# Kernel optimization log

Hardware: AMD Instinct MI355X
Metric: run time of the kernel (lower is better)

Reference implementation:

```python
import jax, jax.numpy as jnp
import numpy as np

HEADS = 8
DIM = 32  # dim_heads


def setup_inputs() -> dict:
    key = jax.random.key(0)
    k1, k2, k3, k4 = jax.random.split(key, 4)
    b, c, h, w = 8, 256, 128, 128
    hidden = HEADS * DIM  # 256
    x = jax.random.normal(k1, (b, c, h, w), dtype=jnp.float32)
    w_qkv = jax.random.normal(k2, (3 * hidden, c), dtype=jnp.float32) * 0.05
    w_out = jax.random.normal(k3, (c, hidden), dtype=jnp.float32) * 0.05
    b_out = jax.random.normal(k4, (c,), dtype=jnp.float32) * 0.05
    return {"x": x, "w_qkv": w_qkv, "w_out": w_out, "b_out": b_out}


def reference(x, w_qkv, w_out, b_out):
    b, c, h, w = x.shape
    n = h * w
    # 1x1 conv == channel matmul: [b, 3*heads*dim, h, w]
    qkv = jnp.einsum('bchw,oc->bohw', x, w_qkv)
    # rearrange 'b (qkv heads c) h w -> qkv b heads c (h w)'
    qkv = qkv.reshape(b, 3, HEADS, DIM, n)
    q, k, v = qkv[:, 0], qkv[:, 1], qkv[:, 2]  # each [b, heads, dim, n]
    k = jax.nn.softmax(k, axis=-1)
    # context: [b, heads, dim, dim]
    context = jnp.einsum('bhdn,bhen->bhde', k, v)
    o = jnp.einsum('bhde,bhdn->bhen', context, q)  # [b, heads, dim, n]
    o = o.reshape(b, HEADS * DIM, h, w)
    # out 1x1 conv with bias
    o = jnp.einsum('bchw,oc->bohw', o, w_out) + b_out[None, :, None, None]
    return o
```

## Files before the change

kernel.cpp:

```cpp
#include <hip/hip_runtime.h>
#include <hip/hip_bf16.h>
#include <cstdint>

#define NPIX 16384
#define BATCH 8
#define CDIM 256

typedef __bf16 bh8 __attribute__((ext_vector_type(8)));
typedef __bf16 bh4 __attribute__((ext_vector_type(4)));
typedef float  fx4 __attribute__((ext_vector_type(4)));

__device__ __forceinline__ void gload16(const void* g, void* l) {
  __builtin_amdgcn_global_load_lds(
      (const __attribute__((address_space(1))) uint32_t*)g,
      (__attribute__((address_space(3))) uint32_t*)l, 16, 0, 0);
}

__device__ __forceinline__ fx4 mfma16(bh8 a, bh8 b, fx4 c) {
  return __builtin_amdgcn_mfma_f32_16x16x32_bf16(a, b, c, 0, 0, 0);
}

__device__ __forceinline__ void pbar() {
  asm volatile("" ::: "memory");
  __builtin_amdgcn_s_barrier();
  asm volatile("" ::: "memory");
}
#define VMWI(n) asm volatile("s_waitcnt vmcnt(" #n ")" ::: "memory")

__global__ __launch_bounds__(256) void prep_w(const float* __restrict__ w_qkv,
                                              __bf16* __restrict__ wqb,
                                              __bf16* __restrict__ wqT) {
  __shared__ float tile[32][33];
  int bid = blockIdx.x;
  if (bid < 512) {
    int i = bid * 256 + threadIdx.x;
    wqb[i] = (__bf16)w_qkv[256 * 256 + i];
  } else {
    bid -= 512;
    const int t0 = (bid & 7) * 32, o0 = (bid >> 3) * 32;
    const int tx = threadIdx.x & 31, ty = threadIdx.x >> 5;
#pragma unroll
    for (int j = 0; j < 4; ++j) {
      int r = ty * 4 + j;
      tile[r][tx] = w_qkv[(size_t)(o0 + r) * 256 + t0 + tx];
    }
    __syncthreads();
#pragma unroll
    for (int j = 0; j < 4; ++j) {
      int tl = ty * 4 + j;
      wqT[(size_t)(t0 + tl) * 256 + o0 + tx] = (__bf16)tile[tx][tl];
    }
  }
}

__global__ __launch_bounds__(256) void transpose_x(const float* __restrict__ x,
                                                   __bf16* __restrict__ xT) {
  __shared__ float tf[64][68];
  const int n0 = blockIdx.x * 64, c0 = blockIdx.y * 64, b = blockIdx.z;
  const int u = threadIdx.x;
#pragma unroll
  for (int i = 0; i < 4; ++i) {
    int j = i * 256 + u;
    int r = j >> 4, q = j & 15;
    *(fx4*)&tf[r][q * 4] =
        *(const fx4*)&x[((size_t)b * CDIM + c0 + r) * NPIX + n0 + q * 4];
  }
  __syncthreads();
  const int nl = u >> 2, cq = (u & 3) * 16;
#pragma unroll
  for (int w = 0; w < 2; ++w) {
    bh8 v;
#pragma unroll
    for (int j = 0; j < 8; ++j) v[j] = (__bf16)tf[cq + w * 8 + j][nl];
    *(bh8*)&xT[((size_t)b * NPIX + n0 + nl) * CDIM + c0 + cq + w * 8] = v;
  }
}


#define BSP(pb) ((__bf16*)(smem + 32768 + (pb)*16384))

#define STA(kt)                                                                \
  do {                                                                         \
    _Pragma("unroll") for (int i_ = 0; i_ < 4; ++i_) {                         \
      int j_ = i_ * 512 + tid;                                                 \
      int row_ = j_ >> 3, c_ = j_ & 7;                                         \
      int sc_ = c_ ^ (row_ & 7);                                               \
      const __bf16* sb_;                                                       \
      if (EPI == 0) sb_ = (i_ < 2) ? Abk + (size_t)row_ * 256                  \
                                   : Abv + (size_t)(row_ - 128) * 256;         \
      else          sb_ = Ab + (size_t)row_ * 256;                             \
      gload16(sb_ + (kt)*64 + sc_ * 8, As + j_ * 8);                           \
    }                                                                          \
  } while (0)

#define STB(kt, pb)                                                            \
  do {                                                                         \
    _Pragma("unroll") for (int i_ = 0; i_ < 2; ++i_) {                         \
      int j_ = i_ * 512 + tid;                                                 \
      int row_ = j_ >> 3, c_ = j_ & 7;                                         \
      int sc_ = c_ ^ (row_ & 7);                                               \
      gload16(Bb + (size_t)row_ * 256 + (kt)*64 + sc_ * 8, BSP(pb) + j_ * 8);  \
    }                                                                          \
  } while (0)

#define COMP(pb)                                                               \
  do {                                                                         \
    _Pragma("unroll") for (int ks_ = 0; ks_ < 2; ++ks_) {                      \
      bh8 a_[4], b_[4];                                                        \
      const int swk_ = (ks_ * 4 + fq) ^ (fr & 7);                              \
      _Pragma("unroll") for (int m_ = 0; m_ < 4; ++m_)                         \
        a_[m_] = *(const bh8*)&As[(wm * 64 + m_ * 16 + fr) * 64 + swk_ * 8];   \
      _Pragma("unroll") for (int n_ = 0; n_ < 4; ++n_)                         \
        b_[n_] = *(const bh8*)&BSP(pb)[(wn * 64 + n_ * 16 + fr) * 64 + swk_ * 8];\
      _Pragma("unroll") for (int m_ = 0; m_ < 4; ++m_)                         \
      _Pragma("unroll") for (int n_ = 0; n_ < 4; ++n_)                         \
        acc[m_][n_] = mfma16(a_[m_], b_[n_], acc[m_][n_]);                     \
    }                                                                          \
  } while (0)

template <int EPI>
__global__ __launch_bounds__(512, 4) void gemm256(
    const __bf16* __restrict__ A, const __bf16* __restrict__ Bx,
    float* __restrict__ S_part, float* __restrict__ Zpart,
    const float* __restrict__ bias, float* __restrict__ fout) {
  __shared__ __align__(16) char smem[66560];
  __bf16* As = (__bf16*)smem;
  const int tid = threadIdx.x;
  const int bx = (EPI == 0) ? blockIdx.y : blockIdx.x;
  const int by = (EPI == 0) ? blockIdx.x : blockIdx.y;
  const int b = blockIdx.z;
  const int lane = tid & 63, wid = tid >> 6;
  const int wm = wid >> 1, wn = wid & 1;
  const int fr = lane & 15, fq = lane >> 4;
  const int hg = by * 4;
  const __bf16* Abk = A + (size_t)(hg * 32) * 256;
  const __bf16* Abv = A + (size_t)(256 + hg * 32) * 256;
  const __bf16* Ab  = A + (size_t)b * 65536;
  const __bf16* Bb = Bx + ((size_t)b * NPIX + (size_t)bx * 128) * 256;

  fx4 acc[4][4] = {};

  STB(0, 0); STA(0);
  STB(1, 1); VMWI(2); pbar(); COMP(0); pbar(); STA(1);
  STB(2, 0); VMWI(2); pbar(); COMP(1); pbar(); STA(2);
  STB(3, 1); VMWI(2); pbar(); COMP(0); pbar(); STA(3);
             VMWI(0); pbar(); COMP(1); pbar();

  if (EPI == 0) {
    float* zrow = (float*)(smem + 65536);
    if (tid < 128) zrow[tid] = 0.f;
#pragma unroll
    for (int m = 0; m < 4; ++m)
#pragma unroll
      for (int n = 0; n < 4; ++n)
#pragma unroll
        for (int j = 0; j < 4; ++j) {
          int r = wm * 64 + m * 16 + fq * 4 + j;
          int px = wn * 64 + n * 16 + fr;
          int pc = px >> 3;
          if (wm < 2) {
            int byo = r * 256 + ((pc ^ (r & 7)) << 4) + (px & 7) * 2;
            *(__bf16*)(smem + byo) = (__bf16)__expf(acc[m][n][j]);
          } else {
            int r2 = r - 128;
            int byo = r2 * 256 + ((pc ^ (r2 & 7)) << 4) + (px & 7) * 2;
            *(__bf16*)(smem + 32768 + byo) = (__bf16)acc[m][n][j];
          }
        }
    __syncthreads();
    {
      int r = tid >> 2, c0 = (tid & 3) * 32;
      float za = 0.f;
#pragma unroll
      for (int i2 = 0; i2 < 4; ++i2) {
        int px0 = c0 + i2 * 8;
        int pc = px0 >> 3;
        bh8 ev = *(const bh8*)(smem + r * 256 + ((pc ^ (r & 7)) << 4));
#pragma unroll
        for (int jj = 0; jj < 8; ++jj) za += (float)ev[jj];
      }
      atomicAdd(&zrow[r], za);
    }
    fx4 sac0 = {}, sac1 = {};
#pragma unroll
    for (int t2 = 0; t2 < 2; ++t2) {
      int tk = wid * 2 + t2;
      int hl = tk >> 2, quad = tk & 3;
      int drow = (quad >> 1) * 16, erow = (quad & 1) * 16;
      fx4 sac = {};
#pragma unroll
      for (int kt2 = 0; kt2 < 4; ++kt2) {
        int ra = hl * 32 + drow + fr;
        int rb = hl * 32 + erow + fr;
        int pc = kt2 * 4 + fq;
        bh8 af = *(const bh8*)(smem + ra * 256 + ((pc ^ (ra & 7)) << 4));
        bh8 bf = *(const bh8*)(smem + 32768 + rb * 256 + ((pc ^ (rb & 7)) << 4));
        sac = mfma16(af, bf, sac);
      }
      if (t2 == 0) sac0 = sac; else sac1 = sac;
    }
    __syncthreads();
    float* Sb = (float*)smem;
#pragma unroll
    for (int t2 = 0; t2 < 2; ++t2) {
      int tk = wid * 2 + t2;
      int hl = tk >> 2, quad = tk & 3;
      int drow = (quad >> 1) * 16, erow = (quad & 1) * 16;
      fx4 sv = (t2 == 0) ? sac0 : sac1;
#pragma unroll
      for (int j = 0; j < 4; ++j)
        Sb[hl * 1024 + (drow + fq * 4 + j) * 32 + erow + fr] = sv[j];
    }
    __syncthreads();
    {
      int hl = tid >> 7, idx = tid & 127;
      float* sp = S_part + ((size_t)((b * 8 + hg + hl) * 128 + bx)) * 1024;
      fx4 v0 = *(const fx4*)&Sb[hl * 1024 + idx * 8];
      fx4 v1 = *(const fx4*)&Sb[hl * 1024 + idx * 8 + 4];
      *(fx4*)&sp[idx * 8] = v0;
      *(fx4*)&sp[idx * 8 + 4] = v1;
      if (hl == 0) {
        float* sp2 = S_part + ((size_t)((b * 8 + hg + 2 + (idx >> 6)) * 128 + bx)) * 1024;
        (void)sp2;
      }
    }
    if (tid < 128) {
      int head = hg + (tid >> 5);
      Zpart[((size_t)(b * 8 + head) * 128 + bx) * 32 + (tid & 31)] = zrow[tid];
    }
  } else {
    const size_t obase = (size_t)b * CDIM * NPIX + (size_t)bx * 128;
    float* Ls = (float*)smem;
#pragma unroll
    for (int m = 0; m < 4; ++m) {
      __syncthreads();
#pragma unroll
      for (int n = 0; n < 4; ++n)
#pragma unroll
        for (int j = 0; j < 4; ++j)
          Ls[(wm * 16 + fq * 4 + j) * 132 + wn * 64 + n * 16 + fr] =
              acc[m][n][j] + bias[wm * 64 + m * 16 + fq * 4 + j];
      __syncthreads();
#pragma unroll
      for (int it = 0; it < 4; ++it) {
        int u = it * 512 + tid;
        int rr = u >> 5, cc = u & 31;
        int gch = (rr >> 4) * 64 + m * 16 + (rr & 15);
        fx4 val = *(const fx4*)&Ls[rr * 132 + cc * 4];
        *(fx4*)&fout[obase + (size_t)gch * NPIX + cc * 4] = val;
      }
    }
  }
}

__global__ __launch_bounds__(256) void reduce_ctx(const float* __restrict__ S_part,
                                                  const float* __restrict__ Zpart,
                                                  float* __restrict__ ctx) {
  const int seg = blockIdx.x;
  const int bh = blockIdx.y;
  const int t = threadIdx.x;
  __shared__ float zs[8];
  if (t < 8) zs[t] = 0.f;
  __syncthreads();
  {
    int row = seg * 8 + (t >> 5);
    float z = 0.f;
    for (int ch = (t & 31); ch < 128; ch += 32)
      z += Zpart[((size_t)bh * 128 + ch) * 32 + row];
    atomicAdd(&zs[t >> 5], z);
  }
  __syncthreads();
  const int i = seg * 256 + t;
  float s = 0.f;
  for (int ch = 0; ch < 128; ++ch) s += S_part[((size_t)bh * 128 + ch) * 1024 + i];
  ctx[(size_t)bh * 1024 + i] = s / zs[t >> 5];
}

__global__ __launch_bounds__(256) void make_w2(const float* __restrict__ ctx,
                                               const float* __restrict__ w_out,
                                               __bf16* __restrict__ W2b) {
  const int oc = blockIdx.x, b = blockIdx.y, t = threadIdx.x;
  const int h = t >> 5, d = t & 31;
  const float* wrow = w_out + oc * 256 + h * 32;
  const float* crow = ctx + (((size_t)b * 8 + h) * 32 + d) * 32;
  float s = 0.f;
#pragma unroll
  for (int e = 0; e < 32; ++e) s += wrow[e] * crow[e];
  W2b[((size_t)b * 256 + oc) * 256 + t] = (__bf16)s;
}

__global__ __launch_bounds__(256) void make_w3(const __bf16* __restrict__ W2b,
                                               const __bf16* __restrict__ wqT,
                                               __bf16* __restrict__ W3) {
  const int bx = blockIdx.x, by = blockIdx.y, b = blockIdx.z;
  const int lane = threadIdx.x & 63, wid = threadIdx.x >> 6;
  const int wm = wid >> 1, wn = wid & 1;
  const int fr = lane & 15, fq = lane >> 4;
  const __bf16* Ab = W2b + (size_t)b * 65536 + (size_t)(by * 128 + wm * 64) * 256;
  const __bf16* Bb = wqT + (size_t)(bx * 128 + wn * 64) * 256;
  fx4 acc[4][4] = {};
#pragma unroll
  for (int h = 0; h < 8; ++h) {
    bh8 a_[4], b_[4];
#pragma unroll
    for (int m = 0; m < 4; ++m)
      a_[m] = *(const bh8*)(Ab + (size_t)(m * 16 + fr) * 256 + h * 32 + fq * 8);
#pragma unroll
    for (int n = 0; n < 4; ++n)
      b_[n] = *(const bh8*)(Bb + (size_t)(n * 16 + fr) * 256 + h * 32 + fq * 8);
#pragma unroll
    for (int m = 0; m < 4; ++m)
#pragma unroll
      for (int n = 0; n < 4; ++n) acc[m][n] = mfma16(a_[m], b_[n], acc[m][n]);
  }
#pragma unroll
  for (int m = 0; m < 4; ++m)
#pragma unroll
    for (int n = 0; n < 4; ++n) {
      int r0 = by * 128 + wm * 64 + m * 16 + fq * 4;
      int t0 = bx * 128 + wn * 64 + n * 16 + fr;
#pragma unroll
      for (int j = 0; j < 4; ++j)
        W3[(size_t)b * 65536 + (size_t)(r0 + j) * 256 + t0] = (__bf16)acc[m][n][j];
    }
}

extern "C" void kernel_launch(void* const* d_in, const int* in_sizes, int n_in,
                              void* d_out, int out_size, void* d_ws, size_t ws_size,
                              hipStream_t stream) {
  const float* x     = (const float*)d_in[0];
  const float* w_qkv = (const float*)d_in[1];
  const float* w_out = (const float*)d_in[2];
  const float* b_out = (const float*)d_in[3];
  float* out = (float*)d_out;

  char* ws = (char*)d_ws;
  __bf16* xT    = (__bf16*)(ws);
  __bf16* wqb   = (__bf16*)(ws + 67108864ull);
  __bf16* wqT   = (__bf16*)(ws + 67371008ull);
  __bf16* W2b   = (__bf16*)(ws + 67502080ull);
  __bf16* W3    = (__bf16*)(ws + 68550656ull);
  float*  S_part= (float*) (ws + 69599232ull);
  float*  Zpart = (float*) (ws + 103153664ull);
  float*  ctx   = (float*) (ws + 104202240ull);

  prep_w<<<576, 256, 0, stream>>>(w_qkv, wqb, wqT);
  transpose_x<<<dim3(NPIX / 64, CDIM / 64, BATCH), 256, 0, stream>>>(x, xT);
  gemm256<0><<<dim3(2, NPIX / 128, BATCH), 512, 0, stream>>>(
      wqb, xT, S_part, Zpart, nullptr, nullptr);
  reduce_ctx<<<dim3(4, 64), 256, 0, stream>>>(S_part, Zpart, ctx);
  make_w2<<<dim3(256, BATCH), 256, 0, stream>>>(ctx, w_out, W2b);
  make_w3<<<dim3(2, 2, BATCH), 256, 0, stream>>>(W2b, wqT, W3);
  gemm256<1><<<dim3(NPIX / 128, 1, BATCH), 512, 0, stream>>>(
      W3, xT, nullptr, nullptr, b_out, out);
}
```

Measured before the change: 177.2 us.

## Replace partial context buffers and reduce kernel with global atomic accumulation

```diff
diff --git a/kernel.cpp b/kernel.cpp
--- a/kernel.cpp
+++ b/kernel.cpp
@@ -29,13 +29,14 @@
 
 __global__ __launch_bounds__(256) void prep_w(const float* __restrict__ w_qkv,
                                               __bf16* __restrict__ wqb,
-                                              __bf16* __restrict__ wqT) {
+                                              __bf16* __restrict__ wqT,
+                                              float* __restrict__ zero_base) {
   __shared__ float tile[32][33];
   int bid = blockIdx.x;
   if (bid < 512) {
     int i = bid * 256 + threadIdx.x;
     wqb[i] = (__bf16)w_qkv[256 * 256 + i];
-  } else {
+  } else if (bid < 576) {
     bid -= 512;
     const int t0 = (bid & 7) * 32, o0 = (bid >> 3) * 32;
     const int tx = threadIdx.x & 31, ty = threadIdx.x >> 5;
@@ -50,6 +51,9 @@
       int tl = ty * 4 + j;
       wqT[(size_t)(t0 + tl) * 256 + o0 + tx] = (__bf16)tile[tx][tl];
     }
+  } else {
+    int i = (bid - 576) * 256 + threadIdx.x;
+    zero_base[i] = 0.f;
   }
 }
 
@@ -121,7 +125,7 @@
 template <int EPI>
 __global__ __launch_bounds__(512, 4) void gemm256(
     const __bf16* __restrict__ A, const __bf16* __restrict__ Bx,
-    float* __restrict__ S_part, float* __restrict__ Zpart,
+    float* __restrict__ ctx_raw, float* __restrict__ Z_raw,
     const float* __restrict__ bias, float* __restrict__ fout) {
   __shared__ __align__(16) char smem[66560];
   __bf16* As = (__bf16*)smem;
@@ -214,19 +218,14 @@
     __syncthreads();
     {
       int hl = tid >> 7, idx = tid & 127;
-      float* sp = S_part + ((size_t)((b * 8 + hg + hl) * 128 + bx)) * 1024;
-      fx4 v0 = *(const fx4*)&Sb[hl * 1024 + idx * 8];
-      fx4 v1 = *(const fx4*)&Sb[hl * 1024 + idx * 8 + 4];
-      *(fx4*)&sp[idx * 8] = v0;
-      *(fx4*)&sp[idx * 8 + 4] = v1;
-      if (hl == 0) {
-        float* sp2 = S_part + ((size_t)((b * 8 + hg + 2 + (idx >> 6)) * 128 + bx)) * 1024;
-        (void)sp2;
-      }
+      float* cr = ctx_raw + (size_t)(b * 8 + hg + hl) * 1024 + idx * 8;
+#pragma unroll
+      for (int j = 0; j < 8; ++j)
+        atomicAdd(&cr[j], Sb[hl * 1024 + idx * 8 + j]);
     }
     if (tid < 128) {
       int head = hg + (tid >> 5);
-      Zpart[((size_t)(b * 8 + head) * 128 + bx) * 32 + (tid & 31)] = zrow[tid];
+      atomicAdd(&Z_raw[(size_t)(b * 8 + head) * 32 + (tid & 31)], zrow[tid]);
     }
   } else {
     const size_t obase = (size_t)b * CDIM * NPIX + (size_t)bx * 128;
@@ -253,40 +252,19 @@
   }
 }
 
-__global__ __launch_bounds__(256) void reduce_ctx(const float* __restrict__ S_part,
-                                                  const float* __restrict__ Zpart,
-                                                  float* __restrict__ ctx) {
-  const int seg = blockIdx.x;
-  const int bh = blockIdx.y;
-  const int t = threadIdx.x;
-  __shared__ float zs[8];
-  if (t < 8) zs[t] = 0.f;
-  __syncthreads();
-  {
-    int row = seg * 8 + (t >> 5);
-    float z = 0.f;
-    for (int ch = (t & 31); ch < 128; ch += 32)
-      z += Zpart[((size_t)bh * 128 + ch) * 32 + row];
-    atomicAdd(&zs[t >> 5], z);
-  }
-  __syncthreads();
-  const int i = seg * 256 + t;
-  float s = 0.f;
-  for (int ch = 0; ch < 128; ++ch) s += S_part[((size_t)bh * 128 + ch) * 1024 + i];
-  ctx[(size_t)bh * 1024 + i] = s / zs[t >> 5];
-}
-
-__global__ __launch_bounds__(256) void make_w2(const float* __restrict__ ctx,
+__global__ __launch_bounds__(256) void make_w2(const float* __restrict__ ctx_raw,
+                                               const float* __restrict__ Z_raw,
                                                const float* __restrict__ w_out,
                                                __bf16* __restrict__ W2b) {
   const int oc = blockIdx.x, b = blockIdx.y, t = threadIdx.x;
   const int h = t >> 5, d = t & 31;
   const float* wrow = w_out + oc * 256 + h * 32;
-  const float* crow = ctx + (((size_t)b * 8 + h) * 32 + d) * 32;
+  const float* crow = ctx_raw + (((size_t)b * 8 + h) * 32 + d) * 32;
+  const float z = Z_raw[((size_t)b * 8 + h) * 32 + d];
   float s = 0.f;
 #pragma unroll
   for (int e = 0; e < 32; ++e) s += wrow[e] * crow[e];
-  W2b[((size_t)b * 256 + oc) * 256 + t] = (__bf16)s;
+  W2b[((size_t)b * 256 + oc) * 256 + t] = (__bf16)(s / z);
 }
 
 __global__ __launch_bounds__(256) void make_w3(const __bf16* __restrict__ W2b,
@@ -335,21 +313,19 @@
   float* out = (float*)d_out;
 
   char* ws = (char*)d_ws;
-  __bf16* xT    = (__bf16*)(ws);
-  __bf16* wqb   = (__bf16*)(ws + 67108864ull);
-  __bf16* wqT   = (__bf16*)(ws + 67371008ull);
-  __bf16* W2b   = (__bf16*)(ws + 67502080ull);
-  __bf16* W3    = (__bf16*)(ws + 68550656ull);
-  float*  S_part= (float*) (ws + 69599232ull);
-  float*  Zpart = (float*) (ws + 103153664ull);
-  float*  ctx   = (float*) (ws + 104202240ull);
-
-  prep_w<<<576, 256, 0, stream>>>(w_qkv, wqb, wqT);
+  __bf16* xT     = (__bf16*)(ws);
+  __bf16* wqb    = (__bf16*)(ws + 67108864ull);
+  __bf16* wqT    = (__bf16*)(ws + 67371008ull);
+  __bf16* W2b    = (__bf16*)(ws + 67502080ull);
+  __bf16* W3     = (__bf16*)(ws + 68550656ull);
+  float*  ctx_raw= (float*) (ws + 69599232ull);
+  float*  Z_raw  = (float*) (ws + 69861376ull);
+
+  prep_w<<<840, 256, 0, stream>>>(w_qkv, wqb, wqT, ctx_raw);
   transpose_x<<<dim3(NPIX / 64, CDIM / 64, BATCH), 256, 0, stream>>>(x, xT);
   gemm256<0><<<dim3(2, NPIX / 128, BATCH), 512, 0, stream>>>(
-      wqb, xT, S_part, Zpart, nullptr, nullptr);
-  reduce_ctx<<<dim3(4, 64), 256, 0, stream>>>(S_part, Zpart, ctx);
-  make_w2<<<dim3(256, BATCH), 256, 0, stream>>>(ctx, w_out, W2b);
+      wqb, xT, ctx_raw, Z_raw, nullptr, nullptr);
+  make_w2<<<dim3(256, BATCH), 256, 0, stream>>>(ctx_raw, Z_raw, w_out, W2b);
   make_w3<<<dim3(2, 2, BATCH), 256, 0, stream>>>(W2b, wqT, W3);
   gemm256<1><<<dim3(NPIX / 128, 1, BATCH), 512, 0, stream>>>(
       W3, xT, nullptr, nullptr, b_out, out);
```

New measurement: 399.2 us. +125.3%, slower.
